# Performance work log

Measured on AMD Instinct MI355X. Metric: run time of the kernel, lower is better.

The kernel has to match this reference:

```python
import jax, jax.numpy as jnp
import numpy as np
from functools import partial

# --- constants from module init / yolov5 NMS conventions ---
CONF_THRES = 0.25
IOU_THRES = 0.45
PATCH_CONF = 0.001
GN = jnp.array([640.0, 640.0, 640.0, 640.0])  # img_size[[1,0,1,0]]
MAX_WH = 4096.0       # per-class NMS offset trick
K_CLEAN = 256         # fixed-size cap for clean detections (max_det=1000 effectively)
K_PATCH = 1024        # fixed-size cap for patch detections (max_det=30000 effectively)
MAXDET_CLEAN = 1000
MAXDET_PATCH = 30000
B, N, NC = 8, 25200, 80


def xywh2xyxy(x):
    xy, wh = x[..., :2], x[..., 2:4]
    return jnp.concatenate([xy - wh * 0.5, xy + wh * 0.5], axis=-1)


def pairwise_iou(a, b):
    # a: [A,4], b: [B,4] -> [A,B] jaccard overlap (same math as IoU.get_iou)
    tl = jnp.maximum(a[:, None, :2], b[None, :, :2])
    br = jnp.minimum(a[:, None, 2:], b[None, :, 2:])
    wh = jnp.clip(br - tl, 0.0)
    inter = wh[..., 0] * wh[..., 1]
    area_a = (a[:, 2] - a[:, 0]) * (a[:, 3] - a[:, 1])
    area_b = (b[:, 2] - b[:, 0]) * (b[:, 3] - b[:, 1])
    return inter / (area_a[:, None] + area_b[None, :] - inter)


def greedy_nms(iou_mat, valid, iou_thres):
    # iou_mat: [K,K] (score-sorted order), valid: [K] bool. Greedy suppression.
    K = valid.shape[0]
    j = jnp.arange(K)

    def body(i, keep):
        suppress = keep[i] & (iou_mat[i] > iou_thres) & (j > i)
        return keep & ~suppress

    return jax.lax.fori_loop(0, K, body, valid)


def _nms_single(pred, conf_thres, K, max_det):
    # pred: [N, 5+nc] raw yolov5 prediction for one image
    boxes = xywh2xyxy(pred[:, :4])
    obj = pred[:, 4]
    cls_scores = pred[:, 5:] * obj[:, None]          # conf = obj * cls
    conf = cls_scores.max(axis=-1)
    cls = jnp.argmax(cls_scores, axis=-1).astype(pred.dtype)
    valid = (obj > conf_thres) & (conf > conf_thres)
    mscore = jnp.where(valid, conf, -1.0)
    _, idx = jax.lax.top_k(mscore, K)                # fixed-size candidate prefilter
    bk, ck, vk = boxes[idx], cls[idx], valid[idx]
    off_boxes = bk + (ck * MAX_WH)[:, None]          # class-offset NMS
    iou = pairwise_iou(off_boxes, off_boxes)
    keep = greedy_nms(jax.lax.stop_gradient(iou), vk, IOU_THRES)
    keep = keep & (jnp.cumsum(keep.astype(jnp.int32)) <= max_det)
    return bk, ck, keep


def _forward(output_clean, output_patch):
    nms_clean = jax.vmap(lambda p: _nms_single(p, CONF_THRES, K_CLEAN, MAXDET_CLEAN))
    nms_patch = jax.vmap(lambda p: _nms_single(p, PATCH_CONF, K_PATCH, MAXDET_PATCH))
    bc, cc, kc = nms_clean(output_clean)   # [B,Kc,4],[B,Kc],[B,Kc]
    bp, cp, kp = nms_patch(output_patch)   # [B,Kp,4],[B,Kp],[B,Kp]
    bc_n = bc / GN
    bp_n = bp / GN

    def per_img(bp_i, cp_i, kp_i, bc_i, cc_i, kc_i):
        iou = pairwise_iou(bp_i, bc_i)                       # [Kp, Kc]
        match = kp_i[:, None] & (cp_i[:, None] == cc_i[None, :])
        tm = jnp.max(jnp.where(match, iou, 0.0), axis=0)     # max IoU per clean det
        return jnp.sum(jnp.where(kc_i, tm, 0.0)), jnp.sum(kc_i.astype(jnp.float32))

    sums, counts = jax.vmap(per_img)(bp_n, cp, kp, bc_n, cc, kc)
    total, cnt = sums.sum(), counts.sum()
    return jnp.where(cnt > 0, 1.0 - total / jnp.maximum(cnt, 1.0), 1.0)


def setup_inputs() -> dict:
    key = jax.random.key(0)
    k1, k2 = jax.random.split(key)

    def make(k):
        kxy, kwh, ko, kc = jax.random.split(k, 4)
        xy = jax.random.uniform(kxy, (B, N, 2)) * 608.0 + 16.0   # centers in-frame
        wh = jax.random.uniform(kwh, (B, N, 2)) * 96.0 + 8.0     # plausible box sizes
        obj = jax.random.uniform(ko, (B, N, 1))
        cls = jax.random.uniform(kc, (B, N, NC))
        return jnp.concatenate([xy, wh, obj, cls], axis=-1)

    return {"output_clean": make(k1), "output_patch": make(k2)}


def reference(output_clean, output_patch):
    return _forward(output_clean, output_patch)
```

## Files before the change

kernel.cpp:

```cpp
#include <hip/hip_runtime.h>

#define N_ANCH 25200
#define NCLS   80
#define ROW    85
#define NIMG   16
#define KMAX   1024
#define NBINS  1024
#define CAND_CAP 4096
#define SC2_RPC 16
#define SC2_CPI 1575
#define SC2_CFLOATS (SC2_RPC*ROW)
#define SC4_BPI 96
#define SC4_WPI 192
#define PCHUNK 64
#define CCNT_STRIDE 16

typedef unsigned long long u64;
typedef unsigned int u32;

#define OFF_KEYS 0ull
#define OFF_HIST 3225600ull
#define OFF_CCNT 3291136ull
#define OFF_CAND 3292160ull
#define OFF_SEL  3816448ull
#define OFF_BOX  3947520ull
#define OFF_CLS  4209664ull
#define OFF_RINIT 4275200ull
#define OFF_KEEP 4277248ull
#define WS_NEED  4342784ull
#define ZERO_BYTES 66560ull

__device__ __forceinline__ int key_bin(u64 key) {
    u32 hi = (u32)(key >> 32);
    if (hi == 0u) return 0;
    float conf = __uint_as_float(hi - 0x40000000u);
    int b = 1 + (int)(conf * 1022.0f);
    return b > 1023 ? 1023 : b;
}

__device__ __forceinline__ u64 readlane64(u64 v, int src) {
    u32 lo = (u32)__builtin_amdgcn_readlane((int)(u32)(v & 0xffffffffull), src);
    u32 hi = (u32)__builtin_amdgcn_readlane((int)(u32)(v >> 32), src);
    return ((u64)hi << 32) | (u64)lo;
}

__device__ __forceinline__ u64 shfl64_xor(u64 v, int m) {
    int lo = __shfl_xor((int)(u32)(v & 0xffffffffull), m, 64);
    int hi = __shfl_xor((int)(u32)(v >> 32), m, 64);
    return ((u64)(u32)hi << 32) | (u64)(u32)lo;
}

#define SC_LOAD6(v0, v1, v2, v3, v4, v5, ch) {                                \
    const float4* _s = (const float4*)(img + (size_t)(ch) * SC2_CFLOATS);     \
    v0 = _s[lane];       v1 = _s[lane + 64];  v2 = _s[lane + 128];            \
    v3 = _s[lane + 192]; v4 = _s[lane + 256];                                 \
    if (lane < 20) v5 = _s[lane + 320];                                       \
}
#define SC_STORE6(v0, v1, v2, v3, v4, v5) {                                   \
    float4* _d = (float4*)buf;                                                \
    _d[lane] = v0;       _d[lane + 64] = v1;  _d[lane + 128] = v2;            \
    _d[lane + 192] = v3; _d[lane + 256] = v4;                                 \
    if (lane < 20) _d[lane + 320] = v5;                                       \
}

__device__ __forceinline__ void sc_compute(int b, int c, int lane, const float* buf,
                                           u64* __restrict__ keys, int* bh)
{
    const int r = lane & 15, h = lane >> 4;
    const float* p = buf + r * ROW;
    const float obj = p[4];
    float best = -1.0f; int bc = 0;
    #pragma unroll
    for (int d = 0; d < 20; ++d) {
        const float s = p[5 + h * 20 + d] * obj;
        if (s > best) { best = s; bc = h * 20 + d; }
    }
    #pragma unroll
    for (int m = 16; m <= 32; m <<= 1) {
        const float o = __shfl_xor(best, m, 64);
        const int  oc = __shfl_xor(bc, m, 64);
        if (o > best || (o == best && oc < bc)) { best = o; bc = oc; }
    }
    if (h == 0) {
        const int n = c * SC2_RPC + r;
        const float th = (b < 8) ? 0.25f : 0.001f;
        const bool valid = (obj > th) && (best > th);
        const u32 hi = valid ? (__float_as_uint(best) + 0x40000000u) : 0u;
        if (valid) {
            int bin = 1 + (int)(best * 1022.0f);
            if (bin > 1023) bin = 1023;
            atomicAdd(&bh[bin], 1);
        }
        const u32 nbar = 32767u - (u32)n;
        keys[(size_t)b * N_ANCH + n] =
            ((u64)hi << 32) | ((u64)nbar << 8) | (u64)(u32)bc;
    }
}

__global__ __launch_bounds__(128, 3) void k_score(const float* __restrict__ clean,
                                                  const float* __restrict__ patch,
                                                  u64* __restrict__ keys,
                                                  int* __restrict__ hist)
{
    __shared__ float lds[2][SC2_CFLOATS];
    __shared__ int bh[NBINS];
    const int t = threadIdx.x;
    const int wv = t >> 6, lane = t & 63;
    const int b = blockIdx.x / SC4_BPI;
    const int blk = blockIdx.x - b * SC4_BPI;
    const int wimg = blk * 2 + wv;
    for (int i = t; i < NBINS; i += 128) bh[i] = 0;
    __syncthreads();
    const float* img = (b < 8) ? clean + (size_t)b * N_ANCH * ROW
                               : patch + (size_t)(b - 8) * N_ANCH * ROW;
    float* buf = &lds[wv][0];
    float4 a0, a1, a2, a3, a4, a5, b0, b1, b2, b3, b4, b5;
    a5 = make_float4(0.f, 0.f, 0.f, 0.f);
    b5 = make_float4(0.f, 0.f, 0.f, 0.f);
    int c = wimg;
    SC_LOAD6(a0, a1, a2, a3, a4, a5, c);
    while (c < SC2_CPI) {
        int cn = c + SC4_WPI;
        if (cn < SC2_CPI) SC_LOAD6(b0, b1, b2, b3, b4, b5, cn);
        __builtin_amdgcn_sched_barrier(0);
        SC_STORE6(a0, a1, a2, a3, a4, a5);
        sc_compute(b, c, lane, buf, keys, bh);
        c = cn;
        if (c >= SC2_CPI) break;
        cn = c + SC4_WPI;
        if (cn < SC2_CPI) SC_LOAD6(a0, a1, a2, a3, a4, a5, cn);
        __builtin_amdgcn_sched_barrier(0);
        SC_STORE6(b0, b1, b2, b3, b4, b5);
        sc_compute(b, c, lane, buf, keys, bh);
        c = cn;
    }
    __syncthreads();
    for (int i = t; i < NBINS; i += 128)
        if (bh[i]) atomicAdd(&hist[b * NBINS + i], bh[i]);
}

__global__ __launch_bounds__(256) void k_compact(const u64* __restrict__ keys,
                                                 const int* __restrict__ hist,
                                                 int* __restrict__ ccnt,
                                                 u64* __restrict__ cand)
{
    __shared__ int arr[256];
    __shared__ int Tsh;
    const int b = blockIdx.x;
    const int t = threadIdx.x;
    const int K = (b < 8) ? 256 : 1024;
    int hh[4];
    hh[0] = hist[b * NBINS + 4 * t + 0];
    hh[1] = hist[b * NBINS + 4 * t + 1];
    hh[2] = hist[b * NBINS + 4 * t + 2];
    hh[3] = hist[b * NBINS + 4 * t + 3];
    const int r = hh[0] + hh[1] + hh[2] + hh[3];
    arr[t] = r;
    __syncthreads();
    for (int off = 1; off < 256; off <<= 1) {
        int v = (t + off < 256) ? arr[t + off] : 0;
        __syncthreads();
        arr[t] += v;
        __syncthreads();
    }
    int cb = arr[t] - r;
    for (int d = 3; d >= 0; --d) {
        int ca = cb + hh[d];
        if (cb < K && ca >= K) Tsh = 4 * t + d;
        cb = ca;
    }
    __syncthreads();
    const int T = Tsh;
    const u64* kp = keys + (size_t)b * N_ANCH;
    const int start = blockIdx.y * 1575;
    const int lane = t & 63;
    #pragma unroll
    for (int it = 0; it < 7; ++it) {
        const int off = it * 256 + t;
        const bool in = off < 1575;
        const u64 key = in ? kp[start + off] : 0ull;
        const bool cnd = in && (key_bin(key) >= T);
        const u64 bal = __ballot(cnd);
        if (bal) {
            int base = 0;
            if (lane == 0) base = atomicAdd(&ccnt[b * CCNT_STRIDE], __popcll(bal));
            base = __shfl(base, 0, 64);
            if (cnd) {
                const int pos = base + __popcll(bal & ((1ull << lane) - 1ull));
                if (pos < CAND_CAP) cand[(size_t)b * CAND_CAP + pos] = key;
            }
        }
    }
}

__global__ __launch_bounds__(1024) void k_sort(const u64* __restrict__ cand,
                                               const int* __restrict__ ccnt,
                                               u64* __restrict__ sel)
{
    __shared__ u64 sk[CAND_CAP];
    const int b = blockIdx.x;
    const int C = min(ccnt[b * CCNT_STRIDE], CAND_CAP);
    const int t = threadIdx.x;
    u64 e0, e1, e2, e3;
    e0 = (t < C) ? cand[(size_t)b * CAND_CAP + t] : 0ull;
    e1 = (1024 + t < C) ? cand[(size_t)b * CAND_CAP + 1024 + t] : 0ull;
    e2 = (2048 + t < C) ? cand[(size_t)b * CAND_CAP + 2048 + t] : 0ull;
    e3 = (3072 + t < C) ? cand[(size_t)b * CAND_CAP + 3072 + t] : 0ull;
    #define CSWAP_D(a, c) { if ((a) < (c)) { u64 _t = (a); (a) = (c); (c) = _t; } }
    #define CSWAP_A(a, c) { if ((a) > (c)) { u64 _t = (a); (a) = (c); (c) = _t; } }
    for (int k = 2; k <= 4096; k <<= 1) {
        for (int j = k >> 1; j > 0; j >>= 1) {
            if (j >= 1024) {
                if (j == 2048) { CSWAP_D(e0, e2); CSWAP_D(e1, e3); }
                else {
                    if (k == 4096) { CSWAP_D(e0, e1); CSWAP_D(e2, e3); }
                    else           { CSWAP_D(e0, e1); CSWAP_A(e2, e3); }
                }
            } else if (j >= 64) {
                __syncthreads();
                sk[t] = e0; sk[1024 + t] = e1; sk[2048 + t] = e2; sk[3072 + t] = e3;
                __syncthreads();
                const int tp = t ^ j;
                #pragma unroll
                for (int p = 0; p < 4; ++p) {
                    const int i = p * 1024 + t;
                    const u64 cv = (p == 0) ? e0 : (p == 1) ? e1 : (p == 2) ? e2 : e3;
                    const u64 o = sk[p * 1024 + tp];
                    const bool take_max = (((i & k) == 0) == ((t & j) == 0));
                    const u64 mx = cv > o ? cv : o;
                    const u64 mn = cv > o ? o : cv;
                    const u64 nv = take_max ? mx : mn;
                    if (p == 0) e0 = nv; else if (p == 1) e1 = nv;
                    else if (p == 2) e2 = nv; else e3 = nv;
                }
            } else {
                #pragma unroll
                for (int p = 0; p < 4; ++p) {
                    const int i = p * 1024 + t;
                    const u64 cv = (p == 0) ? e0 : (p == 1) ? e1 : (p == 2) ? e2 : e3;
                    const u64 o = shfl64_xor(cv, j);
                    const bool take_max = (((i & k) == 0) == ((t & j) == 0));
                    const u64 mx = cv > o ? cv : o;
                    const u64 mn = cv > o ? o : cv;
                    const u64 nv = take_max ? mx : mn;
                    if (p == 0) e0 = nv; else if (p == 1) e1 = nv;
                    else if (p == 2) e2 = nv; else e3 = nv;
                }
            }
        }
    }
    const int K = (b < 8) ? 256 : 1024;
    if (t < K) sel[b * KMAX + t] = e0;
    #undef CSWAP_D
    #undef CSWAP_A
}

__global__ __launch_bounds__(1024) void k_nms_mask(const float* __restrict__ clean,
                                                   const float* __restrict__ patch,
                                                   const u64* __restrict__ sel,
                                                   float4* __restrict__ boxes,
                                                   int* __restrict__ cls,
                                                   u64* __restrict__ rinit,
                                                   u64* __restrict__ mask,
                                                   u64* __restrict__ diag)
{
    __shared__ float4 bx[KMAX];
    __shared__ float ar[KMAX];
    const int b = blockIdx.x, y = blockIdx.y;
    const int K = (b < 8) ? 256 : 1024;
    const int row0 = y * 64;
    if (row0 >= K) return;
    const int t = threadIdx.x;
    {
        const u64 key = (t < K) ? sel[b * KMAX + t] : 0ull;
        const u32 hi = (u32)(key >> 32);
        const bool valid = (t < K) && (hi != 0u);
        const u64 bal = __ballot(valid);
        if (y == 0 && (t & 63) == 0) rinit[b * 16 + (t >> 6)] = ~bal;
        if (t < K) {
            const int n = 32767 - (int)((key >> 8) & 0x7FFFu);
            const int c = (int)(key & 0x7Fu);
            const float* src = ((b < 8) ? (clean + (size_t)b * N_ANCH * ROW)
                                        : (patch + (size_t)(b - 8) * N_ANCH * ROW))
                               + (size_t)n * ROW;
            const float x = src[0], yy = src[1], w = src[2], h = src[3];
            const float4 raw = make_float4(x - w * 0.5f, yy - h * 0.5f,
                                           x + w * 0.5f, yy + h * 0.5f);
            if (y == 0) { boxes[b * KMAX + t] = raw; cls[b * KMAX + t] = c; }
            const float off = (float)c * 4096.0f;
            const float4 ob = make_float4(raw.x + off, raw.y + off,
                                          raw.z + off, raw.w + off);
            bx[t] = ob;
            ar[t] = (ob.z - ob.x) * (ob.w - ob.y);
        }
    }
    __syncthreads();
    const int w   = t >> 6;
    const int row = row0 + (t & 63);
    u64* dst = mask + ((size_t)b * KMAX + row) * 16 + w;
    if (((w << 6) + 63) <= row0 && row0 > 0) { *dst = 0ull; return; }
    const float4 bi = bx[row];
    const float ai = ar[row];
    const int jbase = w << 6;
    u64 m = 0;
    #pragma unroll 8
    for (int k = 0; k < 64; ++k) {
        const int j = jbase + k;
        const float4 bj = bx[j];
        const float ax = fmaxf(bi.x, bj.x), ay = fmaxf(bi.y, bj.y);
        const float bx2 = fminf(bi.z, bj.z), by2 = fminf(bi.w, bj.w);
        const float iw = fmaxf(bx2 - ax, 0.f), ih = fmaxf(by2 - ay, 0.f);
        const float inter = iw * ih;
        const float iou = inter / (ai + ar[j] - inter);
        if (j > row && iou > 0.45f) m |= (1ull << k);
    }
    *dst = m;
    if (w == (row0 >> 6)) diag[(size_t)b * KMAX + row] = m;
}

__global__ __launch_bounds__(1024) void k_nms_scan(const u64* __restrict__ mask,
                                                   const u64* __restrict__ diag,
                                                   const u64* __restrict__ rinit,
                                                   int* __restrict__ keep)
{
    extern __shared__ u64 smem[];
    const int b = blockIdx.x;
    const int K = (b < 8) ? 256 : 1024;
    const int W = K >> 6;
    const int t = threadIdx.x;
    u64* smask = smem;
    u64* sdiag = smem + (size_t)K * 16;
    {
        const float4* s4 = (const float4*)(mask + (size_t)b * KMAX * 16);
        float4* d4 = (float4*)smask;
        const int n4 = (K * 16) >> 1;
        for (int i = t; i < n4; i += 1024) d4[i] = s4[i];
        const float4* s4d = (const float4*)(diag + (size_t)b * KMAX);
        float4* d4d = (float4*)sdiag;
        for (int i = t; i < (K >> 1); i += 1024) d4d[i] = s4d[i];
    }
    __syncthreads();
    if (t >= 64) return;
    const int lane = t;
    const int q = lane >> 4;
    const int wl = lane & 15;
    u64 w_remv = rinit[b * 16 + wl];
    u64 ow = readlane64(w_remv, 0);
    u64 dj = sdiag[lane];
    for (int g = 0; g < W; ++g) {
        u64 nz = __ballot(dj != 0ull);
        u64 o = ow;
        while (nz) {
            const int j = (int)__builtin_ctzll(nz);
            nz &= nz - 1;
            if (!((o >> j) & 1ull)) o |= readlane64(dj, j);
        }
        const u64 kept = ~o;
        if (g + 1 < W) dj = sdiag[(g + 1) * 64 + lane];
        const u64* mrow = smask + (size_t)(g * 64 + q * 16) * 16 + wl;
        const u32 kg = (u32)((kept >> (q * 16)) & 0xFFFFull);
        u64 a0 = 0, a1 = 0;
        #pragma unroll
        for (int i = 0; i < 16; i += 2) {
            const u64 m0 = mrow[(size_t)(i + 0) * 16];
            const u64 m1 = mrow[(size_t)(i + 1) * 16];
            a0 |= ((kg >> i) & 1u) ? m0 : 0ull;
            a1 |= ((kg >> (i + 1)) & 1u) ? m1 : 0ull;
        }
        u64 part = a0 | a1;
        part |= shfl64_xor(part, 16);
        part |= shfl64_xor(part, 32);
        w_remv |= part;
        if (g + 1 < W) ow = readlane64(w_remv, g + 1);
    }
    if (lane < W) {
        #pragma unroll
        for (int k = 0; k < 64; ++k)
            keep[b * KMAX + lane * 64 + k] = (int)(((w_remv >> k) & 1) ^ 1ull);
    }
}

__global__ __launch_bounds__(256) void k_match_partial(const float4* __restrict__ boxes,
                                                       const int* __restrict__ cls,
                                                       const int* __restrict__ keep,
                                                       float* __restrict__ pmax)
{
    __shared__ float4 pb[PCHUNK];
    __shared__ float par[PCHUNK];
    __shared__ int pcls[PCHUNK];
    const int c = blockIdx.x;
    const int p = blockIdx.y;
    const int bp = 8 + c;
    const int t = threadIdx.x;
    if (t < PCHUNK) {
        const int i = p * PCHUNK + t;
        const float4 v = boxes[bp * KMAX + i];
        pb[t] = v;
        par[t] = (v.z - v.x) * (v.w - v.y);
        pcls[t] = keep[bp * KMAX + i] ? cls[bp * KMAX + i] : -1;
    }
    __syncthreads();
    const float4 bc = boxes[c * KMAX + t];
    const int cc = cls[c * KMAX + t];
    const float area_c = (bc.z - bc.x) * (bc.w - bc.y);
    float tm = 0.f;
    #pragma unroll 8
    for (int i = 0; i < PCHUNK; ++i) {
        const float4 bi = pb[i];
        const float ax = fmaxf(bi.x, bc.x), ay = fmaxf(bi.y, bc.y);
        const float bx2 = fminf(bi.z, bc.z), by2 = fminf(bi.w, bc.w);
        const float iw = fmaxf(bx2 - ax, 0.f), ih = fmaxf(by2 - ay, 0.f);
        const float inter = iw * ih;
        const float iou = inter / (par[i] + area_c - inter);
        tm = fmaxf(tm, (pcls[i] == cc) ? iou : 0.f);
    }
    pmax[(c * 16 + p) * 256 + t] = tm;
}

__global__ __launch_bounds__(256) void k_match_final(const float* __restrict__ pmax,
                                                     const int* __restrict__ keep,
                                                     float* __restrict__ out)
{
    __shared__ float red[8];
    const int t = threadIdx.x;
    float tot = 0.f, cn = 0.f;
    for (int c = 0; c < 8; ++c) {
        float tm = 0.f;
        #pragma unroll
        for (int p = 0; p < 16; ++p)
            tm = fmaxf(tm, pmax[(c * 16 + p) * 256 + t]);
        const int kc = keep[c * KMAX + t];
        float val = kc ? tm : 0.f;
        float cv  = kc ? 1.f : 0.f;
        for (int off = 32; off > 0; off >>= 1) {
            val += __shfl_down(val, off);
            cv  += __shfl_down(cv, off);
        }
        const int wv = t >> 6, lane = t & 63;
        if (lane == 0) { red[wv] = val; red[4 + wv] = cv; }
        __syncthreads();
        if (t == 0) {
            tot += red[0] + red[1] + red[2] + red[3];
            cn  += red[4] + red[5] + red[6] + red[7];
        }
        __syncthreads();
    }
    if (t == 0)
        out[0] = (cn > 0.f) ? (1.0f - tot / fmaxf(cn, 1.0f)) : 1.0f;
}

extern "C" void kernel_launch(void* const* d_in, const int* in_sizes, int n_in,
                              void* d_out, int out_size, void* d_ws, size_t ws_size,
                              hipStream_t stream)
{
    if (ws_size < WS_NEED) return;
    const float* clean = (const float*)d_in[0];
    const float* patch = (const float*)d_in[1];
    float* out = (float*)d_out;
    char* ws = (char*)d_ws;

    u64*    keys = (u64*)(ws + OFF_KEYS);
    u64*    mask = (u64*)(ws + OFF_KEYS);
    int*    hist = (int*)(ws + OFF_HIST);
    int*    ccnt = (int*)(ws + OFF_CCNT);
    u64*    cand = (u64*)(ws + OFF_CAND);
    u64*    diag = (u64*)(ws + OFF_CAND);
    float*  pmax = (float*)(ws + OFF_CAND);
    u64*    sel  = (u64*)(ws + OFF_SEL);
    float4* boxes = (float4*)(ws + OFF_BOX);
    int*    cls  = (int*)(ws + OFF_CLS);
    u64*    rinit = (u64*)(ws + OFF_RINIT);
    int*    keep = (int*)(ws + OFF_KEEP);

    hipMemsetAsync(ws + OFF_HIST, 0, ZERO_BYTES, stream);

    k_score<<<NIMG * SC4_BPI, 128, 0, stream>>>(clean, patch, keys, hist);
    k_compact<<<dim3(NIMG, 16), 256, 0, stream>>>(keys, hist, ccnt, cand);
    k_sort<<<NIMG, 1024, 0, stream>>>(cand, ccnt, sel);
    k_nms_mask<<<dim3(NIMG, 16), 1024, 0, stream>>>(clean, patch, sel, boxes, cls,
                                                    rinit, mask, diag);
    k_nms_scan<<<NIMG, 1024, KMAX * 16 * 8 + KMAX * 8, stream>>>(mask, diag, rinit, keep);
    k_match_partial<<<dim3(8, 16), 256, 0, stream>>>(boxes, cls, keep, pmax);
    k_match_final<<<1, 256, 0, stream>>>(pmax, keep, out);
}
```

Baseline: 132.3 us.

## Halve candidate sort capacity and move box gather into sort kernel

Reduces the per-image candidate buffer from 4096 to 2048 entries, so the bitonic sort runs over half as many elements with fewer stages and shared-memory passes. The box decode, class extraction and valid-mask computation move from the NMS mask kernel into the tail of the sort kernel. The mask kernel then reads precomputed boxes instead of having all 16 row-blocks per image gather scattered rows from the raw predictions. If more than 2048 candidates pass the histogram threshold, the extras are dropped and the top-K could differ from the reference.

```diff
diff --git a/kernel.cpp b/kernel.cpp
--- a/kernel.cpp
+++ b/kernel.cpp
@@ -6,7 +6,7 @@
 #define NIMG   16
 #define KMAX   1024
 #define NBINS  1024
-#define CAND_CAP 4096
+#define CAND_CAP 2048
 #define SC2_RPC 16
 #define SC2_CPI 1575
 #define SC2_CFLOATS (SC2_RPC*ROW)
@@ -22,12 +22,12 @@
 #define OFF_HIST 3225600ull
 #define OFF_CCNT 3291136ull
 #define OFF_CAND 3292160ull
-#define OFF_SEL  3816448ull
-#define OFF_BOX  3947520ull
-#define OFF_CLS  4209664ull
-#define OFF_RINIT 4275200ull
-#define OFF_KEEP 4277248ull
-#define WS_NEED  4342784ull
+#define OFF_SEL  3554304ull
+#define OFF_BOX  3685376ull
+#define OFF_CLS  3947520ull
+#define OFF_RINIT 4013056ull
+#define OFF_KEEP 4015104ull
+#define WS_NEED  4080640ull
 #define ZERO_BYTES 66560ull
 
 __device__ __forceinline__ int key_bin(u64 key) {
@@ -195,72 +195,75 @@
 
 __global__ __launch_bounds__(1024) void k_sort(const u64* __restrict__ cand,
                                                const int* __restrict__ ccnt,
-                                               u64* __restrict__ sel)
+                                               const float* __restrict__ clean,
+                                               const float* __restrict__ patch,
+                                               u64* __restrict__ sel,
+                                               float4* __restrict__ boxes,
+                                               int* __restrict__ cls,
+                                               u64* __restrict__ rinit)
 {
     __shared__ u64 sk[CAND_CAP];
     const int b = blockIdx.x;
     const int C = min(ccnt[b * CCNT_STRIDE], CAND_CAP);
     const int t = threadIdx.x;
-    u64 e0, e1, e2, e3;
-    e0 = (t < C) ? cand[(size_t)b * CAND_CAP + t] : 0ull;
-    e1 = (1024 + t < C) ? cand[(size_t)b * CAND_CAP + 1024 + t] : 0ull;
-    e2 = (2048 + t < C) ? cand[(size_t)b * CAND_CAP + 2048 + t] : 0ull;
-    e3 = (3072 + t < C) ? cand[(size_t)b * CAND_CAP + 3072 + t] : 0ull;
-    #define CSWAP_D(a, c) { if ((a) < (c)) { u64 _t = (a); (a) = (c); (c) = _t; } }
-    #define CSWAP_A(a, c) { if ((a) > (c)) { u64 _t = (a); (a) = (c); (c) = _t; } }
-    for (int k = 2; k <= 4096; k <<= 1) {
+    u64 e0 = (t < C) ? cand[(size_t)b * CAND_CAP + t] : 0ull;
+    u64 e1 = (1024 + t < C) ? cand[(size_t)b * CAND_CAP + 1024 + t] : 0ull;
+    for (int k = 2; k <= 2048; k <<= 1) {
         for (int j = k >> 1; j > 0; j >>= 1) {
-            if (j >= 1024) {
-                if (j == 2048) { CSWAP_D(e0, e2); CSWAP_D(e1, e3); }
-                else {
-                    if (k == 4096) { CSWAP_D(e0, e1); CSWAP_D(e2, e3); }
-                    else           { CSWAP_D(e0, e1); CSWAP_A(e2, e3); }
-                }
+            if (j == 1024) {
+                if (e0 < e1) { u64 tmp = e0; e0 = e1; e1 = tmp; }
             } else if (j >= 64) {
                 __syncthreads();
-                sk[t] = e0; sk[1024 + t] = e1; sk[2048 + t] = e2; sk[3072 + t] = e3;
+                sk[t] = e0; sk[1024 + t] = e1;
                 __syncthreads();
                 const int tp = t ^ j;
                 #pragma unroll
-                for (int p = 0; p < 4; ++p) {
+                for (int p = 0; p < 2; ++p) {
                     const int i = p * 1024 + t;
-                    const u64 cv = (p == 0) ? e0 : (p == 1) ? e1 : (p == 2) ? e2 : e3;
+                    const u64 cv = (p == 0) ? e0 : e1;
                     const u64 o = sk[p * 1024 + tp];
                     const bool take_max = (((i & k) == 0) == ((t & j) == 0));
                     const u64 mx = cv > o ? cv : o;
                     const u64 mn = cv > o ? o : cv;
                     const u64 nv = take_max ? mx : mn;
-                    if (p == 0) e0 = nv; else if (p == 1) e1 = nv;
-                    else if (p == 2) e2 = nv; else e3 = nv;
+                    if (p == 0) e0 = nv; else e1 = nv;
                 }
             } else {
                 #pragma unroll
-                for (int p = 0; p < 4; ++p) {
+                for (int p = 0; p < 2; ++p) {
                     const int i = p * 1024 + t;
-                    const u64 cv = (p == 0) ? e0 : (p == 1) ? e1 : (p == 2) ? e2 : e3;
+                    const u64 cv = (p == 0) ? e0 : e1;
                     const u64 o = shfl64_xor(cv, j);
                     const bool take_max = (((i & k) == 0) == ((t & j) == 0));
                     const u64 mx = cv > o ? cv : o;
                     const u64 mn = cv > o ? o : cv;
                     const u64 nv = take_max ? mx : mn;
-                    if (p == 0) e0 = nv; else if (p == 1) e1 = nv;
-                    else if (p == 2) e2 = nv; else e3 = nv;
+                    if (p == 0) e0 = nv; else e1 = nv;
                 }
             }
         }
     }
     const int K = (b < 8) ? 256 : 1024;
-    if (t < K) sel[b * KMAX + t] = e0;
-    #undef CSWAP_D
-    #undef CSWAP_A
-}
-
-__global__ __launch_bounds__(1024) void k_nms_mask(const float* __restrict__ clean,
-                                                   const float* __restrict__ patch,
-                                                   const u64* __restrict__ sel,
-                                                   float4* __restrict__ boxes,
-                                                   int* __restrict__ cls,
-                                                   u64* __restrict__ rinit,
+    const u32 hi = (u32)(e0 >> 32);
+    const bool valid = (t < K) && (hi != 0u);
+    const u64 bal = __ballot(valid);
+    if ((t & 63) == 0) rinit[b * 16 + (t >> 6)] = ~bal;
+    if (t < K) {
+        sel[b * KMAX + t] = e0;
+        const int n = 32767 - (int)((e0 >> 8) & 0x7FFFu);
+        const int c = (int)(e0 & 0x7Fu);
+        const float* src = ((b < 8) ? (clean + (size_t)b * N_ANCH * ROW)
+                                    : (patch + (size_t)(b - 8) * N_ANCH * ROW))
+                           + (size_t)n * ROW;
+        const float x = src[0], y = src[1], w = src[2], h = src[3];
+        boxes[b * KMAX + t] = make_float4(x - w * 0.5f, y - h * 0.5f,
+                                          x + w * 0.5f, y + h * 0.5f);
+        cls[b * KMAX + t] = c;
+    }
+}
+
+__global__ __launch_bounds__(1024) void k_nms_mask(const float4* __restrict__ boxes,
+                                                   const int* __restrict__ cls,
                                                    u64* __restrict__ mask,
                                                    u64* __restrict__ diag)
 {
@@ -271,28 +274,13 @@
     const int row0 = y * 64;
     if (row0 >= K) return;
     const int t = threadIdx.x;
-    {
-        const u64 key = (t < K) ? sel[b * KMAX + t] : 0ull;
-        const u32 hi = (u32)(key >> 32);
-        const bool valid = (t < K) && (hi != 0u);
-        const u64 bal = __ballot(valid);
-        if (y == 0 && (t & 63) == 0) rinit[b * 16 + (t >> 6)] = ~bal;
-        if (t < K) {
-            const int n = 32767 - (int)((key >> 8) & 0x7FFFu);
-            const int c = (int)(key & 0x7Fu);
-            const float* src = ((b < 8) ? (clean + (size_t)b * N_ANCH * ROW)
-                                        : (patch + (size_t)(b - 8) * N_ANCH * ROW))
-                               + (size_t)n * ROW;
-            const float x = src[0], yy = src[1], w = src[2], h = src[3];
-            const float4 raw = make_float4(x - w * 0.5f, yy - h * 0.5f,
-                                           x + w * 0.5f, yy + h * 0.5f);
-            if (y == 0) { boxes[b * KMAX + t] = raw; cls[b * KMAX + t] = c; }
-            const float off = (float)c * 4096.0f;
-            const float4 ob = make_float4(raw.x + off, raw.y + off,
-                                          raw.z + off, raw.w + off);
-            bx[t] = ob;
-            ar[t] = (ob.z - ob.x) * (ob.w - ob.y);
-        }
+    if (t < K) {
+        const float4 raw = boxes[b * KMAX + t];
+        const float off = (float)cls[b * KMAX + t] * 4096.0f;
+        const float4 ob = make_float4(raw.x + off, raw.y + off,
+                                      raw.z + off, raw.w + off);
+        bx[t] = ob;
+        ar[t] = (ob.z - ob.x) * (ob.w - ob.y);
     }
     __syncthreads();
     const int w   = t >> 6;
@@ -476,9 +464,8 @@
 
     k_score<<<NIMG * SC4_BPI, 128, 0, stream>>>(clean, patch, keys, hist);
     k_compact<<<dim3(NIMG, 16), 256, 0, stream>>>(keys, hist, ccnt, cand);
-    k_sort<<<NIMG, 1024, 0, stream>>>(cand, ccnt, sel);
-    k_nms_mask<<<dim3(NIMG, 16), 1024, 0, stream>>>(clean, patch, sel, boxes, cls,
-                                                    rinit, mask, diag);
+    k_sort<<<NIMG, 1024, 0, stream>>>(cand, ccnt, clean, patch, sel, boxes, cls, rinit);
+    k_nms_mask<<<dim3(NIMG, 16), 1024, 0, stream>>>(boxes, cls, mask, diag);
     k_nms_scan<<<NIMG, 1024, KMAX * 16 * 8 + KMAX * 8, stream>>>(mask, diag, rinit, keep);
     k_match_partial<<<dim3(8, 16), 256, 0, stream>>>(boxes, cls, keep, pmax);
     k_match_final<<<1, 256, 0, stream>>>(pmax, keep, out);
```

After: 113.1 us. 1.17x faster.
